# Kernel tuning notes

Hardware: AMD Instinct MI355X
Metric: run time of the kernel (lower is better)

The kernel has to match this reference:

```python
import jax, jax.numpy as jnp
import numpy as np

D_MODEL = 1024
N_HEAD = 16
D_HEAD = 64
D_FF = 4096
X_LEN = 1024
MEM_LEN = 1024
BATCH = 4
TOTAL = MEM_LEN + X_LEN
LN_EPS = 1e-5


def setup_inputs() -> dict:
    key = jax.random.key(0)
    ks = jax.random.split(key, 16)
    inp = {}
    inp["x"] = jax.random.normal(ks[0], (X_LEN, BATCH, D_MODEL), jnp.float32)
    inp["memory"] = jax.random.normal(ks[1], (MEM_LEN, BATCH, D_MODEL), jnp.float32)
    # sinusoidal-style relative position embedding, shape [total, batch, 1, d_model]
    inp["pos_emb"] = jax.random.normal(ks[2], (TOTAL, BATCH, 1, D_MODEL), jnp.float32)
    inp["pos_bias_u"] = jax.random.normal(ks[3], (N_HEAD, D_HEAD), jnp.float32) * 0.02
    inp["pos_bias_v"] = jax.random.normal(ks[4], (N_HEAD, D_HEAD), jnp.float32) * 0.02
    # causal mask with memory: query i may attend to keys j <= i + mem_len
    i = jnp.arange(X_LEN)[:, None]
    j = jnp.arange(TOTAL)[None, :]
    mask2d = j > (i + MEM_LEN)  # True = masked
    inp["mask"] = jnp.broadcast_to(mask2d[:, :, None], (X_LEN, TOTAL, BATCH))
    s = 0.02
    inp["Wq"] = jax.random.normal(ks[5], (D_MODEL, N_HEAD * D_HEAD), jnp.float32) * s
    inp["Wkv"] = jax.random.normal(ks[6], (D_MODEL, 2 * N_HEAD * D_HEAD), jnp.float32) * s
    inp["Wrel"] = jax.random.normal(ks[7], (D_MODEL, N_HEAD * D_HEAD), jnp.float32) * s
    inp["Wo"] = jax.random.normal(ks[8], (N_HEAD * D_HEAD, D_MODEL), jnp.float32) * s
    inp["ln1_g"] = jnp.ones((D_MODEL,), jnp.float32)
    inp["ln1_b"] = jnp.zeros((D_MODEL,), jnp.float32)
    inp["W1"] = jax.random.normal(ks[9], (D_MODEL, D_FF), jnp.float32) * s
    inp["b1"] = jnp.zeros((D_FF,), jnp.float32)
    inp["W2"] = jax.random.normal(ks[10], (D_FF, D_MODEL), jnp.float32) * s
    inp["b2"] = jnp.zeros((D_MODEL,), jnp.float32)
    inp["ln2_g"] = jnp.ones((D_MODEL,), jnp.float32)
    inp["ln2_b"] = jnp.zeros((D_MODEL,), jnp.float32)
    return inp


def _layer_norm(x, g, b):
    mu = jnp.mean(x, axis=-1, keepdims=True)
    var = jnp.var(x, axis=-1, keepdims=True)
    return (x - mu) * jax.lax.rsqrt(var + LN_EPS) * g + b


def _rel_shift(x):
    # x: [I, J, B, N]; faithful to torch _rel_shift (pad dim 1, reinterpret)
    I, J = x.shape[0], x.shape[1]
    zp = jnp.zeros((I, 1) + x.shape[2:], x.dtype)
    xp = jnp.concatenate([zp, x], axis=1)            # [I, J+1, B, N]
    xp = xp.reshape((J + 1, I) + x.shape[2:])        # view as [J+1, I, B, N]
    return xp[1:].reshape(x.shape)


def reference(x, memory, pos_emb, pos_bias_u, pos_bias_v, mask,
              Wq, Wkv, Wrel, Wo, ln1_g, ln1_b, W1, b1, W2, b2, ln2_g, ln2_b):
    scale = 1.0 / (D_HEAD ** 0.5)
    c = jnp.concatenate([memory, x], axis=0)                 # [T, B, D]
    kv = c @ Wkv                                             # [T, B, 2*N*Dh]
    k, v = jnp.split(kv, 2, axis=-1)
    k = k.reshape(TOTAL, BATCH, N_HEAD, D_HEAD)
    v = v.reshape(TOTAL, BATCH, N_HEAD, D_HEAD)
    r = (pos_emb[:, :, 0, :] @ Wrel).reshape(TOTAL, BATCH, N_HEAD, D_HEAD)
    q = (x @ Wq).reshape(X_LEN, BATCH, N_HEAD, D_HEAD)
    qu = q + pos_bias_u
    qv = q + pos_bias_v
    AC = jnp.einsum('ibnd,jbnd->ijbn', qu, k)                # [I, T, B, N]
    BD = _rel_shift(jnp.einsum('ibnd,jbnd->ijbn', qv, r))
    score = (AC + BD) * scale
    score = jnp.where(mask[:, :, :, None], -jnp.inf, score)
    prob = jax.nn.softmax(score, axis=1)                     # softmax over keys (dim 1)
    attn_matrix = prob.mean(axis=(2, 3))                     # [I, T]
    vec = jnp.einsum('ijbn,jbnd->ibnd', prob, v).reshape(X_LEN, BATCH, N_HEAD * D_HEAD)
    attn_out = vec @ Wo
    h = _layer_norm(x + attn_out, ln1_g, ln1_b)
    ff = jax.nn.relu(h @ W1 + b1) @ W2 + b2
    out = _layer_norm(h + ff, ln2_g, ln2_b)
    return out, attn_matrix
```

## Files before the change

kernel.cpp:

```cpp
#include <hip/hip_runtime.h>

#define NHEAD 16
#define DHEAD 64
#define XLEN 1024
#define MEMLEN 1024
#define BATCH 4
#define TOT 2048
#define DFF 4096
#define DM 1024

typedef __attribute__((ext_vector_type(8))) short bf16x8;
typedef __attribute__((ext_vector_type(4))) float f32x4;
typedef __attribute__((ext_vector_type(8))) _Float16 f16x8;
typedef __attribute__((ext_vector_type(4))) _Float16 f16x4;

#define MFB(A, B, C) __builtin_amdgcn_mfma_f32_16x16x32_bf16(A, B, C, 0, 0, 0)
#define MFH(A, B, C) __builtin_amdgcn_mfma_f32_16x16x32_f16(A, B, C, 0, 0, 0)

__device__ __forceinline__ unsigned short bf16rn(float x) {
  union { float f; unsigned u; } c{x};
  unsigned r = c.u + 0x7fffu + ((c.u >> 16) & 1u);
  return (unsigned short)(r >> 16);
}
__device__ __forceinline__ float bf16tof(unsigned short h) {
  union { unsigned u; float f; } c{(unsigned)h << 16};
  return c.f;
}

#define GLOAD_LDS16(gp, lp)                                                    \
  __builtin_amdgcn_global_load_lds(                                            \
      (const __attribute__((address_space(1))) unsigned int*)(gp),             \
      (__attribute__((address_space(3))) unsigned int*)(lp), 16, 0, 0)

__global__ __launch_bounds__(256) void split2_k(
    const float* __restrict__ s0, const float* __restrict__ s1, int splitElems,
    unsigned short* __restrict__ oh, unsigned short* __restrict__ ol)
{
  int i4 = (blockIdx.x * 256 + threadIdx.x) * 4;
  const float* src = (i4 < splitElems) ? (s0 + i4) : (s1 + (i4 - splitElems));
  float4 v = *(const float4*)src;
  ushort4 h, l;
  h.x = bf16rn(v.x); l.x = bf16rn(v.x - bf16tof(h.x));
  h.y = bf16rn(v.y); l.y = bf16rn(v.y - bf16tof(h.y));
  h.z = bf16rn(v.z); l.z = bf16rn(v.z - bf16tof(h.z));
  h.w = bf16rn(v.w); l.w = bf16rn(v.w - bf16tof(h.w));
  *(ushort4*)(oh + i4) = h;
  *(ushort4*)(ol + i4) = l;
}

__global__ __launch_bounds__(256) void tsplit_k(
    const float* __restrict__ W, int K, int N,
    unsigned short* __restrict__ oh, unsigned short* __restrict__ ol)
{
  __shared__ float tile[64][65];
  const int t = threadIdx.x;
  const int bk = blockIdx.x * 64, bn = blockIdx.y * 64;
#pragma unroll
  for (int r = 0; r < 4; ++r) {
    int lr = r * 16 + (t >> 4), lc = (t & 15) * 4;
    *(float4*)&tile[lr][lc] = *(const float4*)&W[(size_t)(bk + lr) * N + bn + lc];
  }
  __syncthreads();
  const int n = t >> 2, kq = t & 3;
  unsigned short* ph = oh + (size_t)(bn + n) * K + bk + kq * 16;
  unsigned short* pl = ol + (size_t)(bn + n) * K + bk + kq * 16;
#pragma unroll
  for (int c = 0; c < 4; ++c) {
    ushort4 h, l;
    float v0 = tile[kq * 16 + c * 4 + 0][n];
    float v1 = tile[kq * 16 + c * 4 + 1][n];
    float v2 = tile[kq * 16 + c * 4 + 2][n];
    float v3 = tile[kq * 16 + c * 4 + 3][n];
    h.x = bf16rn(v0); l.x = bf16rn(v0 - bf16tof(h.x));
    h.y = bf16rn(v1); l.y = bf16rn(v1 - bf16tof(h.y));
    h.z = bf16rn(v2); l.z = bf16rn(v2 - bf16tof(h.z));
    h.w = bf16rn(v3); l.w = bf16rn(v3 - bf16tof(h.w));
    *(ushort4*)(ph + c * 4) = h;
    *(ushort4*)(pl + c * 4) = l;
  }
}

template<int MODE>
__global__ __launch_bounds__(256) void gemm_k(
    const unsigned short* __restrict__ Ah, const unsigned short* __restrict__ Al,
    const unsigned short* __restrict__ Bh, const unsigned short* __restrict__ Bl,
    int N, int K,
    const float* __restrict__ e0, const float* __restrict__ e1,
    float* __restrict__ o0,
    unsigned short* __restrict__ p0, unsigned short* __restrict__ p1,
    unsigned short* __restrict__ p2, unsigned short* __restrict__ p3)
{
  __shared__ unsigned short lds[4][4096];
  const int t = threadIdx.x;
  const int wave = t >> 6, lane = t & 63;
  const int wm = wave >> 1, wn = wave & 1;
  const int m0 = blockIdx.y * 128, n0 = blockIdx.x * 128;

  const unsigned short* gp[2][4];
  unsigned short* lp[2][4];
#pragma unroll
  for (int i = 0; i < 2; ++i) {
    int s = i * 256 + t, row = s >> 2, sl = s & 3;
    int csw = (sl ^ (row & 3)) * 8;
    gp[i][0] = Ah + (size_t)(m0 + row) * K + csw;
    gp[i][1] = Al + (size_t)(m0 + row) * K + csw;
    gp[i][2] = Bh + (size_t)(n0 + row) * K + csw;
    gp[i][3] = Bl + (size_t)(n0 + row) * K + csw;
#pragma unroll
    for (int a = 0; a < 4; ++a) lp[i][a] = &lds[a][s * 8];
  }

  f32x4 acc[4][4] = {};
  const int kg = lane >> 4, r15 = lane & 15;

  for (int k0 = 0; k0 < K; k0 += 32) {
#pragma unroll
    for (int i = 0; i < 2; ++i)
#pragma unroll
      for (int a = 0; a < 4; ++a) GLOAD_LDS16(gp[i][a] + k0, lp[i][a]);
    __syncthreads();

    bf16x8 afh[4], afl[4], bfh[4], bfl[4];
#pragma unroll
    for (int f = 0; f < 4; ++f) {
      int rowA = wm * 64 + f * 16 + r15;
      int ia = (rowA * 4 + (kg ^ (rowA & 3))) * 8;
      afh[f] = *(const bf16x8*)&lds[0][ia];
      afl[f] = *(const bf16x8*)&lds[1][ia];
      int rowB = wn * 64 + f * 16 + r15;
      int ib = (rowB * 4 + (kg ^ (rowB & 3))) * 8;
      bfh[f] = *(const bf16x8*)&lds[2][ib];
      bfl[f] = *(const bf16x8*)&lds[3][ib];
    }
#pragma unroll
    for (int i = 0; i < 4; ++i)
#pragma unroll
      for (int j = 0; j < 4; ++j) {
        acc[i][j] = MFB(afh[i], bfh[j], acc[i][j]);
        acc[i][j] = MFB(afh[i], bfl[j], acc[i][j]);
        acc[i][j] = MFB(afl[i], bfh[j], acc[i][j]);
      }
    __syncthreads();
  }

#pragma unroll
  for (int i = 0; i < 4; ++i)
#pragma unroll
    for (int j = 0; j < 4; ++j)
#pragma unroll
      for (int r = 0; r < 4; ++r) {
        int m = m0 + wm * 64 + i * 16 + kg * 4 + r;
        int nn = n0 + wn * 64 + j * 16 + r15;
        float v = acc[i][j][r];
        if (MODE == 0) {
          int tt = m >> 2, bb = m & 3;
          if (nn < 1024) {
            int hn = nn >> 6, d = nn & 63;
            size_t idx = ((size_t)(bb * 16 + hn) * 2048 + tt) * 64 + d;
            unsigned short hi = bf16rn(v);
            p0[idx] = hi; p1[idx] = bf16rn(v - bf16tof(hi));
          } else {
            int c2 = nn - 1024, hn = c2 >> 6, d = c2 & 63;
            union { _Float16 h; unsigned short u; } cv; cv.h = (_Float16)v;
            p2[((size_t)(bb * 16 + hn) * 64 + d) * 2048 + tt] = cv.u;
          }
        } else if (MODE == 1) {
          int i2 = m >> 2, bb = m & 3;
          int hn = nn >> 6, d = nn & 63;
          size_t idx = ((size_t)(bb * 16 + hn) * 1024 + i2) * 64 + d;
          float vu = v + e0[nn], vv = v + e1[nn];
          unsigned short h0 = bf16rn(vu);
          p0[idx] = h0; p1[idx] = bf16rn(vu - bf16tof(h0));
          unsigned short h1 = bf16rn(vv);
          p2[idx] = h1; p3[idx] = bf16rn(vv - bf16tof(h1));
        } else if (MODE == 2) {
          int tt = m >> 2, bb = m & 3;
          int hn = nn >> 6, d = nn & 63;
          size_t idx = ((size_t)(bb * 16 + hn) * 2048 + tt) * 64 + d;
          unsigned short hi = bf16rn(v);
          p0[idx] = hi; p1[idx] = bf16rn(v - bf16tof(hi));
        } else if (MODE == 3) {
          o0[(size_t)m * N + nn] = v + e0[(size_t)m * N + nn];
        } else if (MODE == 4) {
          float v2 = fmaxf(v + e0[nn], 0.f);
          unsigned short hh = bf16rn(v2);
          p0[(size_t)m * N + nn] = hh;
          p1[(size_t)m * N + nn] = bf16rn(v2 - bf16tof(hh));
        } else if (MODE == 5) {
          o0[(size_t)m * N + nn] = v + e0[nn] + e1[(size_t)m * N + nn];
        }
      }
}

__global__ __launch_bounds__(512, 2) void attn_k(
    const unsigned short* __restrict__ Kh, const unsigned short* __restrict__ Kl,
    const unsigned short* __restrict__ Rh, const unsigned short* __restrict__ Rl,
    const unsigned short* __restrict__ Quh, const unsigned short* __restrict__ Qul,
    const unsigned short* __restrict__ Qvh, const unsigned short* __restrict__ Qvl,
    const _Float16* __restrict__ VT,
    float* __restrict__ vec, float* __restrict__ acc0, float* __restrict__ acc1)
{
  __shared__ _Float16 Dl[16][2072];
  __shared__ unsigned short qs[4][8][16][8];
  __shared__ float red[2][8][16];
  const int t = threadIdx.x, wave = t >> 6, lane = t & 63;
  const int g = lane >> 4, i15 = lane & 15;
  const int i0 = blockIdx.x * 16, b = blockIdx.y;
  const int jr0 = 1008 - i0;
  const int NS = (2048 - jr0) >> 4;
  const int jb = wave * 256;

  f16x4 pacc[16];
#pragma unroll
  for (int js = 0; js < 16; ++js) pacc[js] = (f16x4){};

  for (int hh = 0; hh < 8; ++hh) {
    const int n = blockIdx.z * 8 + hh;
    const size_t bn = (size_t)(b * 16 + n);

    {
      int a = t & 127, arr = t >> 7;
      const unsigned short* sp = arr == 0 ? Quh : arr == 1 ? Qul
                               : arr == 2 ? Qvh : Qvl;
      *(uint4*)&qs[arr][a >> 4][a & 15][0] =
          *(const uint4*)&sp[((bn << 10) + i0 + (a & 15)) * 64 + (a >> 4) * 8];
    }
    __syncthreads();

    for (int s = wave; s < NS; s += 8) {
      const size_t kb = (bn * 2048 + (jr0 + s * 16 + i15)) * 64 + g * 8;
      bf16x8 rh0 = *(const bf16x8*)&Rh[kb];
      bf16x8 rh1 = *(const bf16x8*)&Rh[kb + 32];
      bf16x8 rl0 = *(const bf16x8*)&Rl[kb];
      bf16x8 rl1 = *(const bf16x8*)&Rl[kb + 32];
      bf16x8 vh0 = *(const bf16x8*)&qs[2][g][i15][0];
      bf16x8 vh1 = *(const bf16x8*)&qs[2][4 + g][i15][0];
      bf16x8 vl0 = *(const bf16x8*)&qs[3][g][i15][0];
      bf16x8 vl1 = *(const bf16x8*)&qs[3][4 + g][i15][0];
      f32x4 acc = {};
      acc = MFB(rh0, vh0, acc); acc = MFB(rh1, vh1, acc);
      acc = MFB(rh0, vl0, acc); acc = MFB(rh1, vl1, acc);
      acc = MFB(rl0, vh0, acc); acc = MFB(rl1, vh1, acc);
#pragma unroll
      for (int r = 0; r < 4; ++r)
        Dl[i15][s * 16 + g * 4 + r] = (_Float16)acc[r];
    }
    __syncthreads();

    f32x4 sa[16];
#pragma unroll
    for (int js = 0; js < 16; ++js) sa[js] = (f32x4){};
    {
      bf16x8 uh0 = *(const bf16x8*)&qs[0][g][i15][0];
      bf16x8 uh1 = *(const bf16x8*)&qs[0][4 + g][i15][0];
      bf16x8 ul0 = *(const bf16x8*)&qs[1][g][i15][0];
      bf16x8 ul1 = *(const bf16x8*)&qs[1][4 + g][i15][0];
#pragma unroll 2
      for (int js = 0; js < 16; ++js) {
        const size_t kb = (bn * 2048 + (jb + js * 16 + i15)) * 64 + g * 8;
        bf16x8 kh0 = *(const bf16x8*)&Kh[kb];
        bf16x8 kh1 = *(const bf16x8*)&Kh[kb + 32];
        bf16x8 kl0 = *(const bf16x8*)&Kl[kb];
        bf16x8 kl1 = *(const bf16x8*)&Kl[kb + 32];
        f32x4 a = sa[js];
        a = MFB(kh0, uh0, a); a = MFB(kh1, uh1, a);
        a = MFB(kh0, ul0, a); a = MFB(kh1, ul1, a);
        a = MFB(kl0, uh0, a); a = MFB(kl1, uh1, a);
        sa[js] = a;
      }
    }

    float m = -1e30f;
#pragma unroll
    for (int js = 0; js < 16; ++js)
#pragma unroll
      for (int r = 0; r < 4; ++r) {
        int j = jb + js * 16 + g * 4 + r;
        float sv = (sa[js][r] + (float)Dl[i15][j + 15 - i15]) * 0.125f;
        sv = (j <= i0 + i15 + 1024) ? sv : -1e30f;
        sa[js][r] = sv;
        m = fmaxf(m, sv);
      }
    m = fmaxf(m, __shfl_xor(m, 16));
    m = fmaxf(m, __shfl_xor(m, 32));
    if (g == 0) red[0][wave][i15] = m;
    __syncthreads();
    float mi = red[0][0][i15];
#pragma unroll
    for (int w = 1; w < 8; ++w) mi = fmaxf(mi, red[0][w][i15]);
    float l = 0.f;
#pragma unroll
    for (int js = 0; js < 16; ++js)
#pragma unroll
      for (int r = 0; r < 4; ++r) {
        float p = __expf(sa[js][r] - mi);
        sa[js][r] = p; l += p;
      }
    l += __shfl_xor(l, 16);
    l += __shfl_xor(l, 32);
    if (g == 0) red[1][wave][i15] = l;
    __syncthreads();
    float li = 0.f;
#pragma unroll
    for (int w = 0; w < 8; ++w) li += red[1][w][i15];
    float rinv = 1.f / li;
#pragma unroll
    for (int js = 0; js < 16; ++js) {
      f16x4 pk;
#pragma unroll
      for (int r = 0; r < 4; ++r) pk[r] = (_Float16)(sa[js][r] * rinv);
      *(f16x4*)&Dl[i15][jb + js * 16 + g * 4] = pk;
      pacc[js] += pk;
    }
    __syncthreads();

    f32x4 va[4];
#pragma unroll
    for (int d = 0; d < 4; ++d) va[d] = (f32x4){};
#pragma unroll 2
    for (int kc = 0; kc < 8; ++kc) {
      f16x8 pa = *(const f16x8*)&Dl[i15][jb + kc * 32 + g * 8];
#pragma unroll
      for (int d = 0; d < 4; ++d) {
        f16x8 vb = *(const f16x8*)&VT[(bn * 64 + d * 16 + i15) * 2048 + jb + kc * 32 + g * 8];
        va[d] = MFH(pa, vb, va[d]);
      }
    }
    __syncthreads();
    float* sc2 = (float*)&Dl[0][0];
#pragma unroll
    for (int d = 0; d < 4; ++d)
#pragma unroll
      for (int r = 0; r < 4; ++r)
        sc2[(wave * 16 + g * 4 + r) * 64 + d * 16 + i15] = va[d][r];
    __syncthreads();
    {
      int ii = t >> 5, dp = (t & 31) * 2;
      float s0 = 0.f, s1 = 0.f;
#pragma unroll
      for (int w = 0; w < 8; ++w) {
        s0 += sc2[(w * 16 + ii) * 64 + dp];
        s1 += sc2[(w * 16 + ii) * 64 + dp + 1];
      }
      float* vp = &vec[(((size_t)(i0 + ii) * 4 + b) << 10) + n * 64 + dp];
      vp[0] = s0; vp[1] = s1;
    }
    __syncthreads();
  }

  {
    float* ap = blockIdx.z ? acc1 : acc0;
    float* rp = &ap[((size_t)b * 1024 + i0 + i15) * 2048];
#pragma unroll
    for (int js = 0; js < 16; ++js) {
      float4 o;
      o.x = (float)pacc[js][0]; o.y = (float)pacc[js][1];
      o.z = (float)pacc[js][2]; o.w = (float)pacc[js][3];
      *(float4*)&rp[jb + js * 16 + g * 4] = o;
    }
  }
}

__global__ __launch_bounds__(256) void attnfin_k(const float* __restrict__ a0,
                                                 const float* __restrict__ a1,
                                                 float* __restrict__ out)
{
  size_t idx = (size_t)blockIdx.x * 256 + threadIdx.x;
  const size_t S = (size_t)XLEN * TOT;
  float s = 0.f;
#pragma unroll
  for (int b = 0; b < 4; ++b) s += a0[idx + b * S] + a1[idx + b * S];
  out[idx] = s * (1.0f / 64.0f);
}

template<int SPLIT>
__global__ __launch_bounds__(256) void ln_k(const float* __restrict__ in,
                                            const float* __restrict__ g,
                                            const float* __restrict__ bb,
                                            float* __restrict__ out,
                                            unsigned short* __restrict__ oh,
                                            unsigned short* __restrict__ ol)
{
  __shared__ float rbuf[8];
  const int row = blockIdx.x;
  const int t = threadIdx.x;
  const float* p = in + (size_t)row * DM;
  float4 v = *(const float4*)(p + t * 4);
  float s1 = v.x + v.y + v.z + v.w;
  float s2 = v.x * v.x + v.y * v.y + v.z * v.z + v.w * v.w;
#pragma unroll
  for (int off = 32; off; off >>= 1) {
    s1 += __shfl_xor(s1, off);
    s2 += __shfl_xor(s2, off);
  }
  const int wv = t >> 6, lane = t & 63;
  if (lane == 0) { rbuf[wv] = s1; rbuf[4 + wv] = s2; }
  __syncthreads();
  if (t == 0) {
    float a = rbuf[0] + rbuf[1] + rbuf[2] + rbuf[3];
    float b2 = rbuf[4] + rbuf[5] + rbuf[6] + rbuf[7];
    float mu = a * (1.f / DM);
    float var = b2 * (1.f / DM) - mu * mu;
    rbuf[0] = mu;
    rbuf[1] = rsqrtf(var + 1e-5f);
  }
  __syncthreads();
  float mu = rbuf[0], rs = rbuf[1];
  float4 gv = *(const float4*)(g + t * 4);
  float4 bv = *(const float4*)(bb + t * 4);
  float4 o;
  o.x = (v.x - mu) * rs * gv.x + bv.x;
  o.y = (v.y - mu) * rs * gv.y + bv.y;
  o.z = (v.z - mu) * rs * gv.z + bv.z;
  o.w = (v.w - mu) * rs * gv.w + bv.w;
  *(float4*)(out + (size_t)row * DM + t * 4) = o;
  if (SPLIT) {
    ushort4 h, l;
    h.x = bf16rn(o.x); l.x = bf16rn(o.x - bf16tof(h.x));
    h.y = bf16rn(o.y); l.y = bf16rn(o.y - bf16tof(h.y));
    h.z = bf16rn(o.z); l.z = bf16rn(o.z - bf16tof(h.z));
    h.w = bf16rn(o.w); l.w = bf16rn(o.w - bf16tof(h.w));
    *(ushort4*)(oh + (size_t)row * DM + t * 4) = h;
    *(ushort4*)(ol + (size_t)row * DM + t * 4) = l;
  }
}

extern "C" void kernel_launch(void* const* d_in, const int* in_sizes, int n_in,
                              void* d_out, int out_size, void* d_ws, size_t ws_size,
                              hipStream_t stream) {
  const float* x      = (const float*)d_in[0];
  const float* memory = (const float*)d_in[1];
  const float* pos    = (const float*)d_in[2];
  const float* pbu    = (const float*)d_in[3];
  const float* pbv    = (const float*)d_in[4];
  const float* Wq   = (const float*)d_in[6];
  const float* Wkv  = (const float*)d_in[7];
  const float* Wrel = (const float*)d_in[8];
  const float* Wo   = (const float*)d_in[9];
  const float* ln1g = (const float*)d_in[10];
  const float* ln1b = (const float*)d_in[11];
  const float* W1   = (const float*)d_in[12];
  const float* b1   = (const float*)d_in[13];
  const float* W2   = (const float*)d_in[14];
  const float* b2   = (const float*)d_in[15];
  const float* ln2g = (const float*)d_in[16];
  const float* ln2b = (const float*)d_in[17];

  float* out   = (float*)d_out;
  float* attnm = out + (size_t)XLEN * BATCH * DM;
  float* ws = (float*)d_ws;
  const size_t M1 = 1048576;

  unsigned short* c_h   = (unsigned short*)(ws + 0);
  unsigned short* c_l   = (unsigned short*)(ws + 4 * M1);
  float* pos_f[2] = { ws + 8 * M1, ws + 12 * M1 };
  unsigned short* pos_h = (unsigned short*)pos_f[0];
  unsigned short* pos_l = (unsigned short*)pos_f[1];
  unsigned short* Wkvh  = (unsigned short*)(ws + 16 * M1);
  unsigned short* Wkvl  = (unsigned short*)(ws + 17 * M1);
  unsigned short* Wqh   = (unsigned short*)(ws + 18 * M1);
  unsigned short* Wql   = (unsigned short*)(ws + 18 * M1 + M1 / 2);
  unsigned short* Wrelh = (unsigned short*)(ws + 19 * M1);
  unsigned short* Wrell = (unsigned short*)(ws + 19 * M1 + M1 / 2);
  unsigned short* Rh    = (unsigned short*)(ws + 20 * M1);
  unsigned short* Rl    = (unsigned short*)(ws + 24 * M1);
  unsigned short* Quh   = (unsigned short*)(ws + 28 * M1);
  unsigned short* Qul   = (unsigned short*)(ws + 30 * M1);
  unsigned short* Qvh   = (unsigned short*)(ws + 32 * M1);
  unsigned short* Qvl   = (unsigned short*)(ws + 34 * M1);
  unsigned short* Kh    = (unsigned short*)(ws + 8 * M1);
  unsigned short* Kl    = (unsigned short*)(ws + 12 * M1);
  unsigned short* VTu   = (unsigned short*)(ws + 36 * M1);
  float* attnacc0       = ws + 0;
  float* attnacc1       = ws + 44 * M1;
  float* vec            = ws + 16 * M1;
  unsigned short* vech  = (unsigned short*)(ws + 8 * M1);
  unsigned short* vecl  = (unsigned short*)(ws + 10 * M1);
  unsigned short* W1h   = (unsigned short*)(ws + 12 * M1);
  unsigned short* W1l   = (unsigned short*)(ws + 14 * M1);
  unsigned short* W2h   = (unsigned short*)(ws + 0);
  unsigned short* W2l   = (unsigned short*)(ws + 2 * M1);
  unsigned short* Woh   = (unsigned short*)(ws + 4 * M1);
  unsigned short* Wol   = (unsigned short*)(ws + 4 * M1 + M1 / 2);
  float* t1             = ws + 40 * M1;
  float* h              = ws + 16 * M1;
  unsigned short* hhp   = (unsigned short*)(ws + 20 * M1);
  unsigned short* hlp   = (unsigned short*)(ws + 22 * M1);
  unsigned short* ffph  = (unsigned short*)(ws + 24 * M1);
  unsigned short* ffpl  = (unsigned short*)(ws + 32 * M1);
  float* t2             = ws + 8 * M1;

  split2_k<<<8192, 256, 0, stream>>>(memory, x, MEMLEN * BATCH * DM, c_h, c_l);
  split2_k<<<8192, 256, 0, stream>>>(pos, pos, 1 << 30, pos_h, pos_l);
  tsplit_k<<<dim3(16, 32), 256, 0, stream>>>(Wkv, DM, 2048, Wkvh, Wkvl);
  tsplit_k<<<dim3(16, 16), 256, 0, stream>>>(Wq, DM, 1024, Wqh, Wql);
  tsplit_k<<<dim3(16, 16), 256, 0, stream>>>(Wrel, DM, 1024, Wrelh, Wrell);

  gemm_k<2><<<dim3(8, 64), 256, 0, stream>>>(pos_h, pos_l, Wrelh, Wrell, 1024, DM,
      nullptr, nullptr, nullptr, Rh, Rl, nullptr, nullptr);
  gemm_k<1><<<dim3(8, 32), 256, 0, stream>>>(c_h + 4194304, c_l + 4194304, Wqh, Wql,
      1024, DM, pbu, pbv, nullptr, Quh, Qul, Qvh, Qvl);
  gemm_k<0><<<dim3(16, 64), 256, 0, stream>>>(c_h, c_l, Wkvh, Wkvl, 2048, DM,
      nullptr, nullptr, nullptr, Kh, Kl, VTu, nullptr);
  attn_k<<<dim3(64, 4, 2), 512, 0, stream>>>(Kh, Kl, Rh, Rl, Quh, Qul, Qvh, Qvl,
      (const _Float16*)VTu, vec, attnacc0, attnacc1);
  attnfin_k<<<(XLEN * TOT) / 256, 256, 0, stream>>>(attnacc0, attnacc1, attnm);

  split2_k<<<4096, 256, 0, stream>>>(vec, vec, 1 << 30, vech, vecl);
  tsplit_k<<<dim3(16, 64), 256, 0, stream>>>(W1, DM, DFF, W1h, W1l);
  tsplit_k<<<dim3(64, 16), 256, 0, stream>>>(W2, DFF, 1024, W2h, W2l);
  tsplit_k<<<dim3(16, 16), 256, 0, stream>>>(Wo, DM, 1024, Woh, Wol);

  gemm_k<3><<<dim3(8, 32), 256, 0, stream>>>(vech, vecl, Woh, Wol, 1024, DM,
      x, nullptr, t1, nullptr, nullptr, nullptr, nullptr);
  ln_k<1><<<XLEN * BATCH, 256, 0, stream>>>(t1, ln1g, ln1b, h, hhp, hlp);
  gemm_k<4><<<dim3(32, 32), 256, 0, stream>>>(hhp, hlp, W1h, W1l, DFF, DM,
      b1, nullptr, nullptr, ffph, ffpl, nullptr, nullptr);
  gemm_k<5><<<dim3(8, 32), 256, 0, stream>>>(ffph, ffpl, W2h, W2l, 1024, DFF,
      b2, h, t2, nullptr, nullptr, nullptr, nullptr);
  ln_k<0><<<XLEN * BATCH, 256, 0, stream>>>(t2, ln2g, ln2b, out, nullptr, nullptr);
}
```

Measured before the change: 1.859 ms.

## Stage attention scores in LDS as fp16 and defer softmax normalization

The attention kernel no longer keeps the 16 f32x4 score accumulators live in registers. Scores are scaled and masked inside the QK MFMA loop, and the running max is tracked there too. The masked scores are then written as fp16 to a new 64KB LDS buffer, which holds the exponentials for the PV MFMA. Normalization by 1/l is applied to the PV output instead of to the probabilities, which removes one block-wide barrier. The min-blocks launch bound is dropped and several loops are fully unrolled. Total LDS use is now about 130KB per block, so the kernel likely fits only one 512-thread block per CU instead of two. Storing pre-exp scores in fp16 also adds some rounding error.

```diff
diff --git a/kernel.cpp b/kernel.cpp
--- a/kernel.cpp
+++ b/kernel.cpp
@@ -192,7 +192,7 @@
       }
 }
 
-__global__ __launch_bounds__(512, 2) void attn_k(
+__global__ __launch_bounds__(512) void attn_k(
     const unsigned short* __restrict__ Kh, const unsigned short* __restrict__ Kl,
     const unsigned short* __restrict__ Rh, const unsigned short* __restrict__ Rl,
     const unsigned short* __restrict__ Quh, const unsigned short* __restrict__ Qul,
@@ -201,8 +201,10 @@
     float* __restrict__ vec, float* __restrict__ acc0, float* __restrict__ acc1)
 {
   __shared__ _Float16 Dl[16][2072];
+  __shared__ _Float16 Sl[16][2048];
   __shared__ unsigned short qs[4][8][16][8];
   __shared__ float red[2][8][16];
+  __shared__ float rs[16];
   const int t = threadIdx.x, wave = t >> 6, lane = t & 63;
   const int g = lane >> 4, i15 = lane & 15;
   const int i0 = blockIdx.x * 16, b = blockIdx.y;
@@ -237,50 +239,45 @@
       bf16x8 vh1 = *(const bf16x8*)&qs[2][4 + g][i15][0];
       bf16x8 vl0 = *(const bf16x8*)&qs[3][g][i15][0];
       bf16x8 vl1 = *(const bf16x8*)&qs[3][4 + g][i15][0];
-      f32x4 acc = {};
-      acc = MFB(rh0, vh0, acc); acc = MFB(rh1, vh1, acc);
-      acc = MFB(rh0, vl0, acc); acc = MFB(rh1, vl1, acc);
-      acc = MFB(rl0, vh0, acc); acc = MFB(rl1, vh1, acc);
+      f32x4 dacc = {};
+      dacc = MFB(rh0, vh0, dacc); dacc = MFB(rh1, vh1, dacc);
+      dacc = MFB(rh0, vl0, dacc); dacc = MFB(rh1, vl1, dacc);
+      dacc = MFB(rl0, vh0, dacc); dacc = MFB(rl1, vh1, dacc);
 #pragma unroll
       for (int r = 0; r < 4; ++r)
-        Dl[i15][s * 16 + g * 4 + r] = (_Float16)acc[r];
-    }
-    __syncthreads();
-
-    f32x4 sa[16];
-#pragma unroll
-    for (int js = 0; js < 16; ++js) sa[js] = (f32x4){};
+        Dl[i15][s * 16 + g * 4 + r] = (_Float16)dacc[r];
+    }
+    __syncthreads();
+
+    float m = -1e30f;
     {
       bf16x8 uh0 = *(const bf16x8*)&qs[0][g][i15][0];
       bf16x8 uh1 = *(const bf16x8*)&qs[0][4 + g][i15][0];
       bf16x8 ul0 = *(const bf16x8*)&qs[1][g][i15][0];
       bf16x8 ul1 = *(const bf16x8*)&qs[1][4 + g][i15][0];
-#pragma unroll 2
+#pragma unroll
       for (int js = 0; js < 16; ++js) {
         const size_t kb = (bn * 2048 + (jb + js * 16 + i15)) * 64 + g * 8;
         bf16x8 kh0 = *(const bf16x8*)&Kh[kb];
         bf16x8 kh1 = *(const bf16x8*)&Kh[kb + 32];
         bf16x8 kl0 = *(const bf16x8*)&Kl[kb];
         bf16x8 kl1 = *(const bf16x8*)&Kl[kb + 32];
-        f32x4 a = sa[js];
+        f32x4 a = {};
         a = MFB(kh0, uh0, a); a = MFB(kh1, uh1, a);
         a = MFB(kh0, ul0, a); a = MFB(kh1, ul1, a);
         a = MFB(kl0, uh0, a); a = MFB(kl1, uh1, a);
-        sa[js] = a;
+        f16x4 s4;
+#pragma unroll
+        for (int r = 0; r < 4; ++r) {
+          int j = jb + js * 16 + g * 4 + r;
+          float sv = (a[r] + (float)Dl[i15][j + 15 - i15]) * 0.125f;
+          sv = (j <= i0 + i15 + 1024) ? sv : -1e30f;
+          s4[r] = (_Float16)sv;
+          m = fmaxf(m, sv);
+        }
+        *(f16x4*)&Sl[i15][jb + js * 16 + g * 4] = s4;
       }
     }
-
-    float m = -1e30f;
-#pragma unroll
-    for (int js = 0; js < 16; ++js)
-#pragma unroll
-      for (int r = 0; r < 4; ++r) {
-        int j = jb + js * 16 + g * 4 + r;
-        float sv = (sa[js][r] + (float)Dl[i15][j + 15 - i15]) * 0.125f;
-        sv = (j <= i0 + i15 + 1024) ? sv : -1e30f;
-        sa[js][r] = sv;
-        m = fmaxf(m, sv);
-      }
     m = fmaxf(m, __shfl_xor(m, 16));
     m = fmaxf(m, __shfl_xor(m, 32));
     if (g == 0) red[0][wave][i15] = m;
@@ -288,14 +285,20 @@
     float mi = red[0][0][i15];
 #pragma unroll
     for (int w = 1; w < 8; ++w) mi = fmaxf(mi, red[0][w][i15]);
+
     float l = 0.f;
 #pragma unroll
-    for (int js = 0; js < 16; ++js)
+    for (int js = 0; js < 16; ++js) {
+      f16x4 s4 = *(const f16x4*)&Sl[i15][jb + js * 16 + g * 4];
+      f16x4 e4;
 #pragma unroll
       for (int r = 0; r < 4; ++r) {
-        float p = __expf(sa[js][r] - mi);
-        sa[js][r] = p; l += p;
+        float e = __expf((float)s4[r] - mi);
+        e4[r] = (_Float16)e;
+        l += e;
       }
+      *(f16x4*)&Sl[i15][jb + js * 16 + g * 4] = e4;
+    }
     l += __shfl_xor(l, 16);
     l += __shfl_xor(l, 32);
     if (g == 0) red[1][wave][i15] = l;
@@ -304,22 +307,22 @@
 #pragma unroll
     for (int w = 0; w < 8; ++w) li += red[1][w][i15];
     float rinv = 1.f / li;
+    if (wave == 0 && g == 0) rs[i15] = rinv;
+
 #pragma unroll
     for (int js = 0; js < 16; ++js) {
-      f16x4 pk;
-#pragma unroll
-      for (int r = 0; r < 4; ++r) pk[r] = (_Float16)(sa[js][r] * rinv);
-      *(f16x4*)&Dl[i15][jb + js * 16 + g * 4] = pk;
-      pacc[js] += pk;
-    }
-    __syncthreads();
+      f16x4 e4 = *(const f16x4*)&Sl[i15][jb + js * 16 + g * 4];
+#pragma unroll
+      for (int r = 0; r < 4; ++r)
+        pacc[js][r] += (_Float16)((float)e4[r] * rinv);
+    }
 
     f32x4 va[4];
 #pragma unroll
     for (int d = 0; d < 4; ++d) va[d] = (f32x4){};
-#pragma unroll 2
+#pragma unroll
     for (int kc = 0; kc < 8; ++kc) {
-      f16x8 pa = *(const f16x8*)&Dl[i15][jb + kc * 32 + g * 8];
+      f16x8 pa = *(const f16x8*)&Sl[i15][jb + kc * 32 + g * 8];
 #pragma unroll
       for (int d = 0; d < 4; ++d) {
         f16x8 vb = *(const f16x8*)&VT[(bn * 64 + d * 16 + i15) * 2048 + jb + kc * 32 + g * 8];
@@ -332,7 +335,7 @@
     for (int d = 0; d < 4; ++d)
 #pragma unroll
       for (int r = 0; r < 4; ++r)
-        sc2[(wave * 16 + g * 4 + r) * 64 + d * 16 + i15] = va[d][r];
+        sc2[(wave * 16 + g * 4 + r) * 64 + d * 16 + i15] = va[d][r] * rs[g * 4 + r];
     __syncthreads();
     {
       int ii = t >> 5, dp = (t & 31) * 2;
```

After: 1.568 ms. 15.6% less time.
